# Optimization experiments

Measured on AMD Instinct MI355X. Metric: run time of the kernel, lower is better.

Reference implementation:

```python
import jax, jax.numpy as jnp
import numpy as np

STRICT_MAXIMA_BONUS = 10.0
EPS = 1e-7


def _shifter(x):
    # Edge-replicate pad by 1 in D,H,W (matches F.pad(..., 'replicate')).
    p = jnp.pad(x, ((0, 0), (0, 0), (1, 1), (1, 1), (1, 1)), mode='edge')
    D, H, W = x.shape[2:]
    def s(dd, dh, dw):
        return p[:, :, 1 + dd:1 + dd + D, 1 + dh:1 + dh + H, 1 + dw:1 + dw + W]
    return s


def setup_inputs() -> dict:
    key = jax.random.key(0)
    k1, k2 = jax.random.split(key)
    B, C, D, H, W = 2, 1, 4, 1024, 1024
    x = jax.random.normal(k1, (B, C, D, H, W), dtype=jnp.float32)
    # torch.rand(3,3).abs() noise added (scaled by eps) to every Hessian
    hes_noise = jax.random.uniform(k2, (3, 3), dtype=jnp.float32)
    return {"x": x, "hes_noise": hes_noise}


def _forward(x, hes_noise):
    B, C, D, H, W = x.shape
    s = _shifter(x)
    # --- first-order gradients (kornia spatial_gradient3d, mode='diff';
    #     kernel is depth-flipped before conv, hence gz sign) ---
    gx = 0.5 * (s(0, 0, 1) - s(0, 0, -1))   # d/dW
    gy = 0.5 * (s(0, 1, 0) - s(0, -1, 0))   # d/dH
    gz = 0.5 * (s(-1, 0, 0) - s(1, 0, 0))   # d/dD (depth-flipped kernel)
    b = jnp.stack([gx, gy, gz], axis=-1)     # (B,C,D,H,W,3)
    # --- second-order gradients ---
    dxx = s(0, 0, 1) - 2.0 * x + s(0, 0, -1)
    dyy = s(0, 1, 0) - 2.0 * x + s(0, -1, 0)
    dss = s(1, 0, 0) - 2.0 * x + s(-1, 0, 0)
    dxy = 0.25 * (s(0, -1, -1) - s(0, -1, 1) - s(0, 1, -1) + s(0, 1, 1))
    dys = 0.25 * (s(1, -1, 0) - s(1, 1, 0) - s(-1, -1, 0) + s(-1, 1, 0))
    dxs = 0.25 * (s(1, 0, -1) - s(1, 0, 1) - s(-1, 0, -1) + s(-1, 0, 1))
    Hes = jnp.stack([dxx, dxy, dxs,
                     dxy, dyy, dys,
                     dxs, dys, dss], axis=-1).reshape(B, C, D, H, W, 3, 3)
    Hes = Hes + hes_noise * EPS  # ill-conditioning guard, same noise per voxel
    # --- 3x3x3 strict NMS mask (max_pool3d k=3 s=1 p=1; pad identity = -inf) ---
    pooled = jax.lax.reduce_window(x, -jnp.inf, jax.lax.max,
                                   (1, 1, 3, 3, 3), (1, 1, 1, 1, 1), 'SAME')
    nms_mask = x == pooled
    # --- masked batched 3x3 solve: Hes @ x_solved = b at NMS positions only ---
    eye = jnp.eye(3, dtype=x.dtype)
    Hes_safe = jnp.where(nms_mask[..., None, None], Hes, eye)
    sol = jnp.linalg.solve(Hes_safe, b[..., None])[..., 0]
    x_solved = jnp.where(nms_mask[..., None], sol, 0.0)
    dx = -x_solved
    # discard refinements with offset magnitude > 0.7
    big = jnp.max(jnp.abs(dx), axis=-1, keepdims=True) > 0.7
    dx = jnp.where(big, 0.0, dx)
    # value refinement dy = 0.5 * b^T dx
    dy = 0.5 * jnp.sum(b * dx, axis=-1)
    y_max = x + dy + STRICT_MAXIMA_BONUS * nms_mask.astype(x.dtype)
    # coords: flip (x,y,z)->(d,h,w) channel order, add to integer grid
    dx_res = jnp.moveaxis(dx[..., ::-1], -1, 2)  # (B,C,3,D,H,W)
    gd = jnp.broadcast_to(jnp.arange(D, dtype=x.dtype)[:, None, None], (D, H, W))
    gh = jnp.broadcast_to(jnp.arange(H, dtype=x.dtype)[None, :, None], (D, H, W))
    gw = jnp.broadcast_to(jnp.arange(W, dtype=x.dtype)[None, None, :], (D, H, W))
    grid = jnp.stack([gd, gh, gw], axis=0)       # (3,D,H,W)
    coords_max = grid[None, None] + dx_res       # (B,C,3,D,H,W)
    return coords_max, y_max


def reference(x, hes_noise):
    return _forward(x, hes_noise)
```

## Files before the change

kernel.cpp:

```cpp
#include <hip/hip_runtime.h>

#define EPS_F 1e-7f
#define BONUS 10.0f

__global__ __launch_bounds__(256) void quadinterp3d_kernel(
    const float* __restrict__ x, const float* __restrict__ noise,
    float* __restrict__ out, int B, int D, int H, int W)
{
    int w = blockIdx.x * blockDim.x + threadIdx.x;
    int h = blockIdx.y;
    int bd = blockIdx.z;
    int d = bd % D;
    int b = bd / D;
    if (w >= W) return;

    const long long HW  = (long long)H * W;
    const long long DHW = (long long)D * HW;

    int wm = max(w - 1, 0), wp = min(w + 1, W - 1);
    int hm = max(h - 1, 0), hp = min(h + 1, H - 1);
    int dm = max(d - 1, 0), dp = min(d + 1, D - 1);

    const float* base = x + (long long)b * DHW;

    int ds[3] = {dm, d, dp};
    int hs[3] = {hm, h, hp};
    int wsx[3] = {wm, w, wp};

    float v[3][3][3];
#pragma unroll
    for (int i = 0; i < 3; ++i) {
#pragma unroll
        for (int j = 0; j < 3; ++j) {
            const float* row = base + (long long)ds[i] * HW + (long long)hs[j] * W;
#pragma unroll
            for (int k = 0; k < 3; ++k) v[i][j][k] = row[wsx[k]];
        }
    }

    float c = v[1][1][1];

    float gx = 0.5f * (v[1][1][2] - v[1][1][0]);
    float gy = 0.5f * (v[1][2][1] - v[1][0][1]);
    float gz = 0.5f * (v[0][1][1] - v[2][1][1]);

    float dxx = v[1][1][2] - 2.0f * c + v[1][1][0];
    float dyy = v[1][2][1] - 2.0f * c + v[1][0][1];
    float dss = v[2][1][1] - 2.0f * c + v[0][1][1];
    float dxy = 0.25f * (v[1][0][0] - v[1][0][2] - v[1][2][0] + v[1][2][2]);
    float dys = 0.25f * (v[2][0][1] - v[2][2][1] - v[0][0][1] + v[0][2][1]);
    float dxs = 0.25f * (v[2][1][0] - v[2][1][2] - v[0][1][0] + v[0][1][2]);

    float mx27 = c;
#pragma unroll
    for (int i = 0; i < 3; ++i)
#pragma unroll
        for (int j = 0; j < 3; ++j)
#pragma unroll
            for (int k = 0; k < 3; ++k) mx27 = fmaxf(mx27, v[i][j][k]);
    bool mask = (c == mx27);

    float dx0 = 0.0f, dx1 = 0.0f, dx2 = 0.0f, dy = 0.0f;

    if (mask) {
        float A[3][3];
        float rhs[3];
        A[0][0] = dxx + noise[0] * EPS_F;
        A[0][1] = dxy + noise[1] * EPS_F;
        A[0][2] = dxs + noise[2] * EPS_F;
        A[1][0] = dxy + noise[3] * EPS_F;
        A[1][1] = dyy + noise[4] * EPS_F;
        A[1][2] = dys + noise[5] * EPS_F;
        A[2][0] = dxs + noise[6] * EPS_F;
        A[2][1] = dys + noise[7] * EPS_F;
        A[2][2] = dss + noise[8] * EPS_F;
        rhs[0] = gx; rhs[1] = gy; rhs[2] = gz;

        {
            int p = 0; float am = fabsf(A[0][0]);
            if (fabsf(A[1][0]) > am) { am = fabsf(A[1][0]); p = 1; }
            if (fabsf(A[2][0]) > am) { p = 2; }
            if (p != 0) {
#pragma unroll
                for (int j = 0; j < 3; ++j) { float t = A[0][j]; A[0][j] = A[p][j]; A[p][j] = t; }
                float t = rhs[0]; rhs[0] = rhs[p]; rhs[p] = t;
            }
            float m1 = A[1][0] / A[0][0];
            float m2 = A[2][0] / A[0][0];
            A[1][1] -= m1 * A[0][1]; A[1][2] -= m1 * A[0][2]; rhs[1] -= m1 * rhs[0];
            A[2][1] -= m2 * A[0][1]; A[2][2] -= m2 * A[0][2]; rhs[2] -= m2 * rhs[0];
        }
        {
            if (fabsf(A[2][1]) > fabsf(A[1][1])) {
                float t;
                t = A[1][1]; A[1][1] = A[2][1]; A[2][1] = t;
                t = A[1][2]; A[1][2] = A[2][2]; A[2][2] = t;
                t = rhs[1]; rhs[1] = rhs[2]; rhs[2] = t;
            }
            float m = A[2][1] / A[1][1];
            A[2][2] -= m * A[1][2]; rhs[2] -= m * rhs[1];
        }
        float s2 = rhs[2] / A[2][2];
        float s1 = (rhs[1] - A[1][2] * s2) / A[1][1];
        float s0 = (rhs[0] - A[0][1] * s1 - A[0][2] * s2) / A[0][0];

        dx0 = -s0; dx1 = -s1; dx2 = -s2;
        float amax = fmaxf(fabsf(dx0), fmaxf(fabsf(dx1), fabsf(dx2)));
        if (amax > 0.7f) { dx0 = 0.0f; dx1 = 0.0f; dx2 = 0.0f; }
        dy = 0.5f * (gx * dx0 + gy * dx1 + gz * dx2);
    }

    long long spatial = (long long)d * HW + (long long)h * W + w;
    float* oc = out + (long long)b * 3 * DHW + spatial;
    oc[0]       = (float)d + dx2;
    oc[DHW]     = (float)h + dx1;
    oc[2 * DHW] = (float)w + dx0;
    float* oy = out + (long long)B * 3 * DHW + (long long)b * DHW + spatial;
    oy[0] = c + dy + (mask ? BONUS : 0.0f);
}

extern "C" void kernel_launch(void* const* d_in, const int* in_sizes, int n_in,
                              void* d_out, int out_size, void* d_ws, size_t ws_size,
                              hipStream_t stream) {
    const float* x     = (const float*)d_in[0];
    const float* noise = (const float*)d_in[1];
    float* out = (float*)d_out;

    const int B = 2, D = 4, H = 1024, W = 1024;

    dim3 block(256, 1, 1);
    dim3 grid(W / 256, H, B * D);
    quadinterp3d_kernel<<<grid, block, 0, stream>>>(x, noise, out, B, D, H, W);
}
```

Baseline: 184.4 us.

## Process four voxels per thread with float4 loads, shared column maxima, branchless pivoting

```diff
diff --git a/kernel.cpp b/kernel.cpp
--- a/kernel.cpp
+++ b/kernel.cpp
@@ -7,116 +7,142 @@
     const float* __restrict__ x, const float* __restrict__ noise,
     float* __restrict__ out, int B, int D, int H, int W)
 {
-    int w = blockIdx.x * blockDim.x + threadIdx.x;
-    int h = blockIdx.y;
-    int bd = blockIdx.z;
-    int d = bd % D;
-    int b = bd / D;
-    if (w >= W) return;
+    const int d = blockIdx.x;
+    const int h = blockIdx.y;
+    const int b = blockIdx.z;
+    const int w0 = (int)threadIdx.x * 4;
 
-    const long long HW  = (long long)H * W;
-    const long long DHW = (long long)D * HW;
+    const int HW  = H * W;
+    const int DHW = D * HW;
 
-    int wm = max(w - 1, 0), wp = min(w + 1, W - 1);
-    int hm = max(h - 1, 0), hp = min(h + 1, H - 1);
-    int dm = max(d - 1, 0), dp = min(d + 1, D - 1);
+    const int dm = max(d - 1, 0), dp = min(d + 1, D - 1);
+    const int hm = max(h - 1, 0), hp = min(h + 1, H - 1);
+    const int wl = max(w0 - 1, 0);
+    const int wr = min(w0 + 4, W - 1);
 
-    const float* base = x + (long long)b * DHW;
+    const float* base = x + (size_t)b * DHW;
+    const int doffs[3] = { dm * HW, d * HW, dp * HW };
+    const int hoffs[3] = { hm * W,  h * W,  hp * W  };
 
-    int ds[3] = {dm, d, dp};
-    int hs[3] = {hm, h, hp};
-    int wsx[3] = {wm, w, wp};
-
-    float v[3][3][3];
+    float r[3][3][6];
 #pragma unroll
     for (int i = 0; i < 3; ++i) {
 #pragma unroll
         for (int j = 0; j < 3; ++j) {
-            const float* row = base + (long long)ds[i] * HW + (long long)hs[j] * W;
-#pragma unroll
-            for (int k = 0; k < 3; ++k) v[i][j][k] = row[wsx[k]];
+            const float* p = base + (doffs[i] + hoffs[j]);
+            const float4 cv = *reinterpret_cast<const float4*>(p + w0);
+            r[i][j][0] = p[wl];
+            r[i][j][1] = cv.x;
+            r[i][j][2] = cv.y;
+            r[i][j][3] = cv.z;
+            r[i][j][4] = cv.w;
+            r[i][j][5] = p[wr];
         }
     }
 
-    float c = v[1][1][1];
+    const float n0 = noise[0]*EPS_F, n1 = noise[1]*EPS_F, n2 = noise[2]*EPS_F;
+    const float n3 = noise[3]*EPS_F, n4 = noise[4]*EPS_F, n5 = noise[5]*EPS_F;
+    const float n6 = noise[6]*EPS_F, n7 = noise[7]*EPS_F, n8 = noise[8]*EPS_F;
 
-    float gx = 0.5f * (v[1][1][2] - v[1][1][0]);
-    float gy = 0.5f * (v[1][2][1] - v[1][0][1]);
-    float gz = 0.5f * (v[0][1][1] - v[2][1][1]);
-
-    float dxx = v[1][1][2] - 2.0f * c + v[1][1][0];
-    float dyy = v[1][2][1] - 2.0f * c + v[1][0][1];
-    float dss = v[2][1][1] - 2.0f * c + v[0][1][1];
-    float dxy = 0.25f * (v[1][0][0] - v[1][0][2] - v[1][2][0] + v[1][2][2]);
-    float dys = 0.25f * (v[2][0][1] - v[2][2][1] - v[0][0][1] + v[0][2][1]);
-    float dxs = 0.25f * (v[2][1][0] - v[2][1][2] - v[0][1][0] + v[0][1][2]);
-
-    float mx27 = c;
+    float colmax[6];
 #pragma unroll
-    for (int i = 0; i < 3; ++i)
+    for (int k = 0; k < 6; ++k) {
+        float m = r[0][0][k];
 #pragma unroll
-        for (int j = 0; j < 3; ++j)
+        for (int i = 0; i < 3; ++i)
 #pragma unroll
-            for (int k = 0; k < 3; ++k) mx27 = fmaxf(mx27, v[i][j][k]);
-    bool mask = (c == mx27);
-
-    float dx0 = 0.0f, dx1 = 0.0f, dx2 = 0.0f, dy = 0.0f;
-
-    if (mask) {
-        float A[3][3];
-        float rhs[3];
-        A[0][0] = dxx + noise[0] * EPS_F;
-        A[0][1] = dxy + noise[1] * EPS_F;
-        A[0][2] = dxs + noise[2] * EPS_F;
-        A[1][0] = dxy + noise[3] * EPS_F;
-        A[1][1] = dyy + noise[4] * EPS_F;
-        A[1][2] = dys + noise[5] * EPS_F;
-        A[2][0] = dxs + noise[6] * EPS_F;
-        A[2][1] = dys + noise[7] * EPS_F;
-        A[2][2] = dss + noise[8] * EPS_F;
-        rhs[0] = gx; rhs[1] = gy; rhs[2] = gz;
-
-        {
-            int p = 0; float am = fabsf(A[0][0]);
-            if (fabsf(A[1][0]) > am) { am = fabsf(A[1][0]); p = 1; }
-            if (fabsf(A[2][0]) > am) { p = 2; }
-            if (p != 0) {
-#pragma unroll
-                for (int j = 0; j < 3; ++j) { float t = A[0][j]; A[0][j] = A[p][j]; A[p][j] = t; }
-                float t = rhs[0]; rhs[0] = rhs[p]; rhs[p] = t;
-            }
-            float m1 = A[1][0] / A[0][0];
-            float m2 = A[2][0] / A[0][0];
-            A[1][1] -= m1 * A[0][1]; A[1][2] -= m1 * A[0][2]; rhs[1] -= m1 * rhs[0];
-            A[2][1] -= m2 * A[0][1]; A[2][2] -= m2 * A[0][2]; rhs[2] -= m2 * rhs[0];
-        }
-        {
-            if (fabsf(A[2][1]) > fabsf(A[1][1])) {
-                float t;
-                t = A[1][1]; A[1][1] = A[2][1]; A[2][1] = t;
-                t = A[1][2]; A[1][2] = A[2][2]; A[2][2] = t;
-                t = rhs[1]; rhs[1] = rhs[2]; rhs[2] = t;
-            }
-            float m = A[2][1] / A[1][1];
-            A[2][2] -= m * A[1][2]; rhs[2] -= m * rhs[1];
-        }
-        float s2 = rhs[2] / A[2][2];
-        float s1 = (rhs[1] - A[1][2] * s2) / A[1][1];
-        float s0 = (rhs[0] - A[0][1] * s1 - A[0][2] * s2) / A[0][0];
-
-        dx0 = -s0; dx1 = -s1; dx2 = -s2;
-        float amax = fmaxf(fabsf(dx0), fmaxf(fabsf(dx1), fabsf(dx2)));
-        if (amax > 0.7f) { dx0 = 0.0f; dx1 = 0.0f; dx2 = 0.0f; }
-        dy = 0.5f * (gx * dx0 + gy * dx1 + gz * dx2);
+            for (int j = 0; j < 3; ++j) m = fmaxf(m, r[i][j][k]);
+        colmax[k] = m;
     }
 
-    long long spatial = (long long)d * HW + (long long)h * W + w;
-    float* oc = out + (long long)b * 3 * DHW + spatial;
-    oc[0]       = (float)d + dx2;
-    oc[DHW]     = (float)h + dx1;
-    oc[2 * DHW] = (float)w + dx0;
-    float* oy = out + (long long)B * 3 * DHW + (long long)b * DHW + spatial;
-    oy[0] = c + dy + (mask ? BONUS : 0.0f);
+    float od0[4], od1[4], od2[4], oyv[4];
+
+#pragma unroll
+    for (int q = 0; q < 4; ++q) {
+        const float c = r[1][1][q + 1];
+
+        const float gx = 0.5f * (r[1][1][q+2] - r[1][1][q]);
+        const float gy = 0.5f * (r[1][2][q+1] - r[1][0][q+1]);
+        const float gz = 0.5f * (r[0][1][q+1] - r[2][1][q+1]);
+
+        const float dxx = r[1][1][q+2] - 2.0f * c + r[1][1][q];
+        const float dyy = r[1][2][q+1] - 2.0f * c + r[1][0][q+1];
+        const float dss = r[2][1][q+1] - 2.0f * c + r[0][1][q+1];
+        const float dxy = 0.25f * (r[1][0][q] - r[1][0][q+2] - r[1][2][q] + r[1][2][q+2]);
+        const float dys = 0.25f * (r[2][0][q+1] - r[2][2][q+1] - r[0][0][q+1] + r[0][2][q+1]);
+        const float dxs = 0.25f * (r[2][1][q] - r[2][1][q+2] - r[0][1][q] + r[0][1][q+2]);
+
+        const float mx = fmaxf(fmaxf(colmax[q], colmax[q+1]), colmax[q+2]);
+        const bool mask = (c == mx);
+
+        float dx0 = 0.0f, dx1 = 0.0f, dx2 = 0.0f, dy = 0.0f;
+        if (mask) {
+            const float A00 = dxx + n0, A01 = dxy + n1, A02 = dxs + n2;
+            const float A10 = dxy + n3, A11 = dyy + n4, A12 = dys + n5;
+            const float A20 = dxs + n6, A21 = dys + n7, A22 = dss + n8;
+            const float r0 = gx, r1 = gy, r2 = gz;
+
+            const float a0 = fabsf(A00), a1 = fabsf(A10), a2 = fabsf(A20);
+            const bool p2 = a2 > fmaxf(a0, a1);
+            const bool p1 = (a1 > a0) && !p2;
+
+            const float t00 = p1 ? A10 : (p2 ? A20 : A00);
+            const float t01 = p1 ? A11 : (p2 ? A21 : A01);
+            const float t02 = p1 ? A12 : (p2 ? A22 : A02);
+            const float tr0 = p1 ? r1  : (p2 ? r2  : r0);
+            const float u10 = p1 ? A00 : A10;
+            const float u11 = p1 ? A01 : A11;
+            const float u12 = p1 ? A02 : A12;
+            const float ur1 = p1 ? r0  : r1;
+            const float u20 = p2 ? A00 : A20;
+            const float u21 = p2 ? A01 : A21;
+            const float u22 = p2 ? A02 : A22;
+            const float ur2 = p2 ? r0  : r2;
+
+            const float m1 = u10 / t00;
+            const float m2 = u20 / t00;
+            const float e11 = u11 - m1 * t01;
+            const float e12 = u12 - m1 * t02;
+            const float er1 = ur1 - m1 * tr0;
+            const float e21 = u21 - m2 * t01;
+            const float e22 = u22 - m2 * t02;
+            const float er2 = ur2 - m2 * tr0;
+
+            const bool q2 = fabsf(e21) > fabsf(e11);
+            const float f11 = q2 ? e21 : e11;
+            const float f12 = q2 ? e22 : e12;
+            const float fr1 = q2 ? er2 : er1;
+            const float g21 = q2 ? e11 : e21;
+            const float g22 = q2 ? e12 : e22;
+            const float gr2 = q2 ? er1 : er2;
+
+            const float mm  = g21 / f11;
+            const float h22 = g22 - mm * f12;
+            const float hr2 = gr2 - mm * fr1;
+
+            const float s2 = hr2 / h22;
+            const float s1 = (fr1 - f12 * s2) / f11;
+            const float s0 = (tr0 - t01 * s1 - t02 * s2) / t00;
+
+            dx0 = -s0; dx1 = -s1; dx2 = -s2;
+            const float amax = fmaxf(fabsf(dx0), fmaxf(fabsf(dx1), fabsf(dx2)));
+            if (amax > 0.7f) { dx0 = 0.0f; dx1 = 0.0f; dx2 = 0.0f; }
+            dy = 0.5f * (gx * dx0 + gy * dx1 + gz * dx2);
+        }
+
+        od0[q] = (float)d + dx2;
+        od1[q] = (float)h + dx1;
+        od2[q] = (float)(w0 + q) + dx0;
+        oyv[q] = c + dy + (mask ? BONUS : 0.0f);
+    }
+
+    const size_t spatial = (size_t)d * HW + (size_t)h * W + w0;
+    float* oc = out + (size_t)b * 3 * DHW + spatial;
+    *reinterpret_cast<float4*>(oc)                   = make_float4(od0[0], od0[1], od0[2], od0[3]);
+    *reinterpret_cast<float4*>(oc + DHW)             = make_float4(od1[0], od1[1], od1[2], od1[3]);
+    *reinterpret_cast<float4*>(oc + 2 * (size_t)DHW) = make_float4(od2[0], od2[1], od2[2], od2[3]);
+    float* oy = out + (size_t)B * 3 * DHW + (size_t)b * DHW + spatial;
+    *reinterpret_cast<float4*>(oy)                   = make_float4(oyv[0], oyv[1], oyv[2], oyv[3]);
 }
 
 extern "C" void kernel_launch(void* const* d_in, const int* in_sizes, int n_in,
@@ -129,6 +155,6 @@
     const int B = 2, D = 4, H = 1024, W = 1024;
 
     dim3 block(256, 1, 1);
-    dim3 grid(W / 256, H, B * D);
+    dim3 grid(D, H, B);
     quadinterp3d_kernel<<<grid, block, 0, stream>>>(x, noise, out, B, D, H, W);
 }
```

New measurement: 191.9 us. 1.04x slower.
